# Kernel tuning notes

Hardware: AMD Instinct MI355X
Metric: run time of the kernel (lower is better)

Reference implementation:

```python
import jax, jax.numpy as jnp
import numpy as np

LR = 1e-3  # Oja online learning rate
B, D, H, O = 2048, 784, 256, 10


def setup_inputs() -> dict:
    key = jax.random.key(0)
    k0, k1, k2, k3, k4 = jax.random.split(key, 5)
    x = jax.random.normal(k0, (B, D), dtype=jnp.float32)
    whiten_mean = 0.1 * jax.random.normal(k1, (D,), dtype=jnp.float32)
    # whitening matrix ~ identity + small perturbation (well-conditioned)
    whiten_mat = jnp.eye(D, dtype=jnp.float32) + 0.01 * jax.random.normal(k2, (D, D), dtype=jnp.float32)
    oja_W = (1.0 / np.sqrt(D)) * jax.random.normal(k3, (H, D), dtype=jnp.float32)
    readout_W = (1.0 / np.sqrt(H)) * jax.random.normal(k4, (O, H), dtype=jnp.float32)
    readout_b = jnp.zeros((O,), dtype=jnp.float32)
    return {"x": x, "whiten_mean": whiten_mean, "whiten_mat": whiten_mat,
            "oja_W": oja_W, "readout_W": readout_W, "readout_b": readout_b}


def reference(x, whiten_mean, whiten_mat, oja_W, readout_W, readout_b):
    # Whitening transform per sample: x_w = M (x - mu)
    xw = (x - whiten_mean) @ whiten_mat.T  # [B, D]

    # Sequential Oja online updates: y_i = W_i x_i ; W_{i+1} = W_i + lr*(y x^T - (y y^T) W_i)
    def step(W, xi):
        y = W @ xi                                        # [H]
        W_new = W + LR * (jnp.outer(y, xi) - jnp.outer(y, y) @ W)
        return W_new, y

    _, feats = jax.lax.scan(step, oja_W, xw)              # feats: [B, H]

    # dropout(p=0.2) in eval mode is identity; then ReLU and linear readout
    feats = jax.nn.relu(feats)
    logits = feats @ readout_W.T + readout_b              # [B, O]
    return logits
```

## Files before the change

### kernel.cpp

```cpp
#include <hip/hip_runtime.h>

#define LRATE 1e-3f
static constexpr int Bn = 2048;
static constexpr int Dn = 784;
static constexpr int Hn = 256;
static constexpr int On = 10;
static constexpr int Cc = 64;
static constexpr int NCHUNK = Bn / Cc;

static constexpr int AS = 68;
static constexpr int YS = 260;
static constexpr int MSZ = 64 * AS;

__device__ __forceinline__ float red4(float s) {
  s += __uint_as_float(__builtin_amdgcn_mov_dpp(__float_as_uint(s), 0xB1, 0xF, 0xF, true));
  s += __uint_as_float(__builtin_amdgcn_mov_dpp(__float_as_uint(s), 0x4E, 0xF, 0xF, true));
  return s;
}

__global__ __launch_bounds__(256) void whiten_kernel(
    const float* __restrict__ x, const float* __restrict__ mean,
    const float* __restrict__ Mw, float* __restrict__ xw)
{
  __shared__ __align__(16) float As[16][64];
  __shared__ __align__(16) float Bs[16][64];
  const int tid = threadIdx.x;
  const int b0 = blockIdx.x * 64;
  const int d0 = blockIdx.y * 64;
  const int mrow = tid >> 2;
  const int kq = (tid & 3) << 2;
  const int ty = tid >> 4, tx = tid & 15;

  float acc[4][4];
#pragma unroll
  for (int i = 0; i < 4; ++i)
#pragma unroll
    for (int j = 0; j < 4; ++j) acc[i][j] = 0.f;

  for (int k0 = 0; k0 < Dn; k0 += 16) {
    __syncthreads();
    {
      const float4 av = *(const float4*)&x[(b0 + mrow) * Dn + k0 + kq];
      const float4 mv = *(const float4*)&mean[k0 + kq];
      As[kq + 0][mrow] = av.x - mv.x;
      As[kq + 1][mrow] = av.y - mv.y;
      As[kq + 2][mrow] = av.z - mv.z;
      As[kq + 3][mrow] = av.w - mv.w;
      float4 bv = make_float4(0.f, 0.f, 0.f, 0.f);
      if (d0 + mrow < Dn) bv = *(const float4*)&Mw[(d0 + mrow) * Dn + k0 + kq];
      Bs[kq + 0][mrow] = bv.x;
      Bs[kq + 1][mrow] = bv.y;
      Bs[kq + 2][mrow] = bv.z;
      Bs[kq + 3][mrow] = bv.w;
    }
    __syncthreads();
#pragma unroll
    for (int k = 0; k < 16; ++k) {
      const float4 a = *(const float4*)&As[k][ty << 2];
      const float4 b = *(const float4*)&Bs[k][tx << 2];
      acc[0][0] += a.x * b.x; acc[0][1] += a.x * b.y; acc[0][2] += a.x * b.z; acc[0][3] += a.x * b.w;
      acc[1][0] += a.y * b.x; acc[1][1] += a.y * b.y; acc[1][2] += a.y * b.z; acc[1][3] += a.y * b.w;
      acc[2][0] += a.z * b.x; acc[2][1] += a.z * b.y; acc[2][2] += a.z * b.z; acc[2][3] += a.z * b.w;
      acc[3][0] += a.w * b.x; acc[3][1] += a.w * b.y; acc[3][2] += a.w * b.z; acc[3][3] += a.w * b.w;
    }
  }
  const int col = d0 + (tx << 2);
  if (col < Dn) {
#pragma unroll
    for (int i = 0; i < 4; ++i) {
      const int row = b0 + (ty << 2) + i;
      *(float4*)&xw[row * Dn + col] =
          make_float4(acc[i][0], acc[i][1], acc[i][2], acc[i][3]);
    }
  }
}

__global__ __launch_bounds__(256) void sgram_kernel(
    const float* __restrict__ xw, float* __restrict__ S_all)
{
  __shared__ __align__(16) float Xs[64 * 396];
  const int t = threadIdx.x;
  const int c = blockIdx.x;
  const float* xc = xw + (size_t)c * Cc * Dn;
  const int ti = t >> 4, tj = t & 15;
  float acc[4][4];
#pragma unroll
  for (int a = 0; a < 4; ++a)
#pragma unroll
    for (int b = 0; b < 4; ++b) acc[a][b] = 0.f;

  for (int pass = 0; pass < 2; ++pass) {
    __syncthreads();
    for (int e4 = t; e4 < 64 * 98; e4 += 256) {
      const int r = e4 / 98, c4 = e4 - r * 98;
      *(float4*)&Xs[r * 396 + 4 * c4] =
          *(const float4*)&xc[r * Dn + pass * 392 + 4 * c4];
    }
    __syncthreads();
    for (int k4 = 0; k4 < 98; ++k4) {
      float4 A[4], Bv[4];
#pragma unroll
      for (int a = 0; a < 4; ++a) A[a] = *(const float4*)&Xs[(4 * ti + a) * 396 + 4 * k4];
#pragma unroll
      for (int b = 0; b < 4; ++b) Bv[b] = *(const float4*)&Xs[(4 * tj + b) * 396 + 4 * k4];
#pragma unroll
      for (int a = 0; a < 4; ++a)
#pragma unroll
        for (int b = 0; b < 4; ++b)
          acc[a][b] += A[a].x * Bv[b].x + A[a].y * Bv[b].y + A[a].z * Bv[b].z + A[a].w * Bv[b].w;
    }
  }
  float* Sc = S_all + (size_t)c * Cc * Cc;
#pragma unroll
  for (int a = 0; a < 4; ++a)
#pragma unroll
    for (int b = 0; b < 4; ++b)
      Sc[(4 * ti + a) * Cc + 4 * tj + b] = acc[a][b];
}

__global__ __launch_bounds__(256) void yhat_kernel(
    const float* __restrict__ xc, const float* __restrict__ W,
    float* __restrict__ yhat)
{
  const int t = threadIdx.x;
  const int r = t & 63, hh = t >> 6;
  const int h = blockIdx.x * 4 + hh;
  const float4* xr = (const float4*)&xc[r * Dn];
  const float4* wr = (const float4*)&W[h * Dn];
  float acc = 0.f;
#pragma unroll 4
  for (int f = 0; f < 196; ++f) {
    const float4 a = xr[f], b = wr[f];
    acc += a.x * b.x + a.y * b.y + a.z * b.z + a.w * b.w;
  }
  yhat[r * Hn + h] = acc;
}

__global__ __launch_bounds__(256, 1) void seq_kernel(
    const float* __restrict__ yhat_g, const float* __restrict__ S_g,
    float* __restrict__ feats_c, float* __restrict__ beta_g)
{
  __shared__ __align__(16) float lds[8 * MSZ + 1872];
  float* Gy  = lds + 0 * MSZ;
  float* AlT = lds + 1 * MSZ;
  float* BeT = lds + 2 * MSZ;
  float* GuT = lds + 3 * MSZ;
  float* Qs  = lds + 4 * MSZ;
  float* Ts  = lds + 5 * MSZ;
  float* Ss  = lds + 6 * MSZ;
  float* Al  = lds + 7 * MSZ;
  float* VOb = lds + 8 * MSZ;
  float* VMb = VOb + 4 * AS;
  float* GVo = VMb + 4 * AS;
  float* Pk  = GVo + 16;

  const int t = threadIdx.x;
  const int k = t >> 2, qr = t & 3;
  const int m0q = qr * 16;

  for (int e4 = t; e4 < 5 * MSZ / 4; e4 += 256)
    *(float4*)&lds[4 * e4] = make_float4(0.f, 0.f, 0.f, 0.f);
  for (int e4 = t; e4 < 1024; e4 += 256) {
    const int r = e4 >> 4, c4 = e4 & 15;
    *(float4*)&Ss[r * AS + 4 * c4] = ((const float4*)S_g)[e4];
  }
  {
    const int ti = t >> 4, tj = t & 15;
    float acc[4][4];
#pragma unroll
    for (int a = 0; a < 4; ++a)
#pragma unroll
      for (int b = 0; b < 4; ++b) acc[a][b] = 0.f;
    for (int k4 = 0; k4 < 64; ++k4) {
      float4 A[4], Bv[4];
#pragma unroll
      for (int a = 0; a < 4; ++a) A[a] = *(const float4*)&yhat_g[(4 * ti + a) * Hn + 4 * k4];
#pragma unroll
      for (int b = 0; b < 4; ++b) Bv[b] = *(const float4*)&yhat_g[(4 * tj + b) * Hn + 4 * k4];
#pragma unroll
      for (int a = 0; a < 4; ++a)
#pragma unroll
        for (int b = 0; b < 4; ++b)
          acc[a][b] += A[a].x * Bv[b].x + A[a].y * Bv[b].y + A[a].z * Bv[b].z + A[a].w * Bv[b].w;
    }
#pragma unroll
    for (int a = 0; a < 4; ++a)
#pragma unroll
      for (int b = 0; b < 4; ++b)
        Ts[(4 * ti + a) * AS + 4 * tj + b] = acc[a][b];
  }
  __syncthreads();

  __builtin_amdgcn_s_setprio(1);

  for (int b = 0; b < Cc / 4; ++b) {
    const int b0 = 4 * b;
    const int wseg = (b0 + 15) >> 4;
    const int o4 = qr * wseg;

    float4 gyS[4], atS[4], qS[4];
    {
      const float4* gyp = (const float4*)&Gy[k * AS] + o4;
      const float4* atp = (const float4*)&AlT[k * AS] + o4;
      const float4* qp  = (const float4*)&Qs[k * AS] + o4;
#pragma unroll
      for (int f = 0; f < 4; ++f)
        if (f < wseg) { gyS[f] = gyp[f]; atS[f] = atp[f]; qS[f] = qp[f]; }
    }
    float og[4], oq[4], oa[4], grow[4];
#pragma unroll
    for (int s = 0; s < 4; ++s) {
      const float4* pR = (const float4*)&GuT[(b0 + s) * AS] + o4;
      float g0 = 0.f, g1 = 0.f, g2 = 0.f, g3 = 0.f;
      float a0 = 0.f, a1 = 0.f, a2 = 0.f, a3 = 0.f;
      float w0 = 0.f, w1 = 0.f, w2 = 0.f, w3 = 0.f;
#pragma unroll
      for (int f = 0; f < 4; ++f)
        if (f < wseg) {
          const float4 p = pR[f];
          g0 += p.x * gyS[f].x; g1 += p.y * gyS[f].y; g2 += p.z * gyS[f].z; g3 += p.w * gyS[f].w;
          a0 += p.x * atS[f].x; a1 += p.y * atS[f].y; a2 += p.z * atS[f].z; a3 += p.w * atS[f].w;
          w0 += p.x * qS[f].x;  w1 += p.y * qS[f].y;  w2 += p.z * qS[f].z;  w3 += p.w * qS[f].w;
        }
      og[s] = red4((g0 + g1) + (g2 + g3));
      oa[s] = red4((a0 + a1) + (a2 + a3));
      oq[s] = red4((w0 + w1) + (w2 + w3));
      grow[s] = Gy[(b0 + s) * AS + k];
    }
    if (qr == 0)      *(float4*)&Pk[k * 20 + 0] = make_float4(og[0], og[1], og[2], og[3]);
    else if (qr == 1) *(float4*)&Pk[k * 20 + 4] = make_float4(oq[0], oq[1], oq[2], oq[3]);
    else if (qr == 2) *(float4*)&Pk[k * 20 + 8] = make_float4(oa[0], oa[1], oa[2], oa[3]);
    else {
      float vo[4];
#pragma unroll
      for (int s = 0; s < 4; ++s) vo[s] = grow[s] + LRATE * oq[s];
      *(float4*)&Pk[k * 20 + 12] = make_float4(vo[0], vo[1], vo[2], vo[3]);
#pragma unroll
      for (int s = 0; s < 4; ++s) VOb[s * AS + k] = vo[s];
    }
    __syncthreads();

    if (t < 64) {
      const int pr = t >> 2;
      const int sp = pr >> 2, s2 = pr & 3;
      const int q2 = t & 3;
      const float4* gr = (const float4*)&GuT[(b0 + sp) * AS] + q2 * wseg;
      const float4* vr = (const float4*)&VOb[s2 * AS] + q2 * wseg;
      float d0 = 0.f, d1 = 0.f, d2 = 0.f, d3 = 0.f;
#pragma unroll
      for (int f = 0; f < 4; ++f)
        if (f < wseg) {
          const float4 g = gr[f], v = vr[f];
          d0 += g.x * v.x; d1 += g.y * v.y; d2 += g.z * v.z; d3 += g.w * v.w;
        }
      const float d = red4((d0 + d1) + (d2 + d3));
      if (q2 == 0) GVo[pr] = d;
    }
    __syncthreads();

    float T8[4][4], S8v[4][4], OG8[4][4], OQ8[4][4], GV8[4][4];
#pragma unroll
    for (int j = 0; j < 4; ++j) {
      const float4 t4 = *(const float4*)&Ts[(b0 + j) * AS + b0];
      T8[j][0] = t4.x; T8[j][1] = t4.y; T8[j][2] = t4.z; T8[j][3] = t4.w;
      const float4 s4 = *(const float4*)&Ss[(b0 + j) * AS + b0];
      S8v[j][0] = s4.x; S8v[j][1] = s4.y; S8v[j][2] = s4.z; S8v[j][3] = s4.w;
      const float4 g4 = *(const float4*)&Pk[(b0 + j) * 20 + 0];
      OG8[0][j] = g4.x; OG8[1][j] = g4.y; OG8[2][j] = g4.z; OG8[3][j] = g4.w;
      const float4 q4 = *(const float4*)&Pk[(b0 + j) * 20 + 4];
      OQ8[0][j] = q4.x; OQ8[1][j] = q4.y; OQ8[2][j] = q4.z; OQ8[3][j] = q4.w;
      const float4 v4 = ((const float4*)GVo)[j];
      GV8[j][0] = v4.x; GV8[j][1] = v4.y; GV8[j][2] = v4.z; GV8[j][3] = v4.w;
    }
    float G8[4][4], V8[4][4], U8[4][4], W8[4][4], Qd[4];
#pragma unroll
    for (int j = 0; j < 4; ++j) {
      G8[0][j] = T8[0][j] + LRATE * OG8[0][j];
      V8[0][j] = 0.f;
      W8[j][0] = GV8[j][0];
    }
#pragma unroll
    for (int j = 0; j < 4; ++j) U8[0][j] = S8v[0][j] - G8[0][j] - LRATE * W8[j][0];
    Qd[0] = G8[0][0] + LRATE * W8[0][0];
    {
      const float p0 = U8[0][1];
#pragma unroll
      for (int j = 0; j < 4; ++j) G8[1][j] = T8[1][j] + LRATE * (OG8[1][j] + p0 * G8[0][j]);
      V8[1][0] = G8[0][1] + LRATE * (OQ8[1][0] + p0 * Qd[0]);
      V8[1][1] = V8[1][2] = V8[1][3] = 0.f;
#pragma unroll
      for (int j = 0; j < 4; ++j) W8[j][1] = GV8[j][1] + LRATE * (p0 * W8[j][0]);
#pragma unroll
      for (int j = 0; j < 4; ++j)
        U8[1][j] = S8v[1][j] - G8[1][j] - LRATE * (W8[j][1] + V8[1][0] * U8[0][j]);
      Qd[1] = G8[1][1] + LRATE * (W8[1][1] + p0 * V8[1][0]);
    }
    {
      const float p0 = U8[0][2], p1 = U8[1][2];
#pragma unroll
      for (int j = 0; j < 4; ++j)
        G8[2][j] = T8[2][j] + LRATE * (OG8[2][j] + p0 * G8[0][j] + p1 * G8[1][j]);
      V8[2][0] = G8[0][2] + LRATE * (OQ8[2][0] + p0 * Qd[0] + p1 * V8[1][0]);
      V8[2][1] = G8[1][2] + LRATE * (OQ8[2][1] + p1 * Qd[1]);
      V8[2][2] = V8[2][3] = 0.f;
#pragma unroll
      for (int j = 0; j < 4; ++j) W8[j][2] = GV8[j][2] + LRATE * (p0 * W8[j][0] + p1 * W8[j][1]);
#pragma unroll
      for (int j = 0; j < 4; ++j)
        U8[2][j] = S8v[2][j] - G8[2][j] -
                   LRATE * (W8[j][2] + V8[2][0] * U8[0][j] + V8[2][1] * U8[1][j]);
      Qd[2] = G8[2][2] + LRATE * (W8[2][2] + p0 * V8[2][0] + p1 * V8[2][1]);
    }
    {
      const float p0 = U8[0][3], p1 = U8[1][3], p2 = U8[2][3];
#pragma unroll
      for (int j = 0; j < 4; ++j)
        G8[3][j] = T8[3][j] + LRATE * (OG8[3][j] + p0 * G8[0][j] + p1 * G8[1][j] + p2 * G8[2][j]);
      V8[3][0] = G8[0][3] + LRATE * (OQ8[3][0] + p0 * Qd[0] + p1 * V8[1][0] + p2 * V8[2][0]);
      V8[3][1] = G8[1][3] + LRATE * (OQ8[3][1] + p1 * Qd[1] + p2 * V8[2][1]);
      V8[3][2] = G8[2][3] + LRATE * (OQ8[3][2] + p2 * Qd[2]);
      V8[3][3] = 0.f;
#pragma unroll
      for (int j = 0; j < 4; ++j)
        W8[j][3] = GV8[j][3] + LRATE * (p0 * W8[j][0] + p1 * W8[j][1] + p2 * W8[j][2]);
#pragma unroll
      for (int j = 0; j < 4; ++j)
        U8[3][j] = S8v[3][j] - G8[3][j] -
                   LRATE * (W8[j][3] + V8[3][0] * U8[0][j] + V8[3][1] * U8[1][j] +
                            V8[3][2] * U8[2][j]);
      Qd[3] = G8[3][3] + LRATE * (W8[3][3] + p0 * V8[3][0] + p1 * V8[3][1] + p2 * V8[3][2]);
    }

    float TsK[4], OGk[4], OAk[4], VOk[4];
    {
      const float4 tk4 = *(const float4*)&Ts[k * AS + b0];
      TsK[0] = tk4.x; TsK[1] = tk4.y; TsK[2] = tk4.z; TsK[3] = tk4.w;
      const float4 og4 = *(const float4*)&Pk[k * 20 + 0];
      OGk[0] = og4.x; OGk[1] = og4.y; OGk[2] = og4.z; OGk[3] = og4.w;
      const float4 oa4 = *(const float4*)&Pk[k * 20 + 8];
      OAk[0] = oa4.x; OAk[1] = oa4.y; OAk[2] = oa4.z; OAk[3] = oa4.w;
      const float4 vo4 = *(const float4*)&Pk[k * 20 + 12];
      VOk[0] = vo4.x; VOk[1] = vo4.y; VOk[2] = vo4.z; VOk[3] = vo4.w;
    }
    float gy[4], aI[4], vm[4];
    gy[0] = TsK[0] + LRATE * OGk[0];
    { const float a = LRATE * OAk[0]; aI[0] = (k < b0) ? a : ((k == b0) ? 1.f : 0.f); }
    vm[0] = (k < b0) ? VOk[0] : 0.f;
    {
      const float p0 = U8[0][1];
      gy[1] = TsK[1] + LRATE * (OGk[1] + p0 * gy[0]);
      const float a = LRATE * (OAk[1] + p0 * aI[0]);
      aI[1] = (k < b0 + 1) ? a : ((k == b0 + 1) ? 1.f : 0.f);
      const float vt0 = (k == b0) ? Qd[0] : vm[0];
      float v = VOk[1] + LRATE * (p0 * vt0);
      if (k == b0) v += G8[0][1];
      vm[1] = (k < b0 + 1) ? v : 0.f;
    }
    {
      const float p0 = U8[0][2], p1 = U8[1][2];
      gy[2] = TsK[2] + LRATE * (OGk[2] + p0 * gy[0] + p1 * gy[1]);
      const float a = LRATE * (OAk[2] + p0 * aI[0] + p1 * aI[1]);
      aI[2] = (k < b0 + 2) ? a : ((k == b0 + 2) ? 1.f : 0.f);
      const float vt0 = (k == b0) ? Qd[0] : vm[0];
      const float vt1 = (k == b0 + 1) ? Qd[1] : vm[1];
      float v = VOk[2] + LRATE * (p0 * vt0 + p1 * vt1);
      if (k == b0) v += G8[0][2];
      else if (k == b0 + 1) v += G8[1][2];
      vm[2] = (k < b0 + 2) ? v : 0.f;
    }
    {
      const float p0 = U8[0][3], p1 = U8[1][3], p2 = U8[2][3];
      gy[3] = TsK[3] + LRATE * (OGk[3] + p0 * gy[0] + p1 * gy[1] + p2 * gy[2]);
      const float a = LRATE * (OAk[3] + p0 * aI[0] + p1 * aI[1] + p2 * aI[2]);
      aI[3] = (k < b0 + 3) ? a : ((k == b0 + 3) ? 1.f : 0.f);
      const float vt0 = (k == b0) ? Qd[0] : vm[0];
      const float vt1 = (k == b0 + 1) ? Qd[1] : vm[1];
      const float vt2 = (k == b0 + 2) ? Qd[2] : vm[2];
      float v = VOk[3] + LRATE * (p0 * vt0 + p1 * vt1 + p2 * vt2);
      if (k == b0) v += G8[0][3];
      else if (k == b0 + 1) v += G8[1][3];
      else if (k == b0 + 2) v += G8[2][3];
      vm[3] = (k < b0 + 3) ? v : 0.f;
    }
    float qw[4];
#pragma unroll
    for (int s = 0; s < 4; ++s) qw[s] = (k == b0 + s) ? Qd[s] : vm[s];
    if (qr == 0) {
      *(float4*)&Gy[k * AS + b0] = make_float4(gy[0], gy[1], gy[2], gy[3]);
#pragma unroll
      for (int s = 0; s < 4; ++s) Qs[(b0 + s) * AS + k] = qw[s];
    } else if (qr == 1) {
      *(float4*)&AlT[k * AS + b0] = make_float4(aI[0], aI[1], aI[2], aI[3]);
      *(float4*)&Qs[k * AS + b0] = make_float4(qw[0], qw[1], qw[2], qw[3]);
    } else if (qr == 2) {
#pragma unroll
      for (int s = 0; s < 4; ++s) Al[(b0 + s) * AS + k] = aI[s];
#pragma unroll
      for (int s = 0; s < 4; ++s) VMb[s * AS + k] = (k < b0) ? vm[s] : 0.f;
    }
    __syncthreads();

    float4 beS[4], guS[4];
    {
      const float4* bep = (const float4*)&BeT[k * AS] + o4;
      const float4* gup = (const float4*)&GuT[k * AS] + o4;
#pragma unroll
      for (int f = 0; f < 4; ++f)
        if (f < wseg) { beS[f] = bep[f]; guS[f] = gup[f]; }
    }
    float bO[4], gO[4];
#pragma unroll
    for (int s = 0; s < 4; ++s) {
      const float4* vmr = (const float4*)&VMb[s * AS] + o4;
      float b0a = 0.f, b1a = 0.f, b2a = 0.f, b3a = 0.f;
      float u0 = 0.f, u1 = 0.f, u2 = 0.f, u3 = 0.f;
#pragma unroll
      for (int f = 0; f < 4; ++f)
        if (f < wseg) {
          const float4 v = vmr[f];
          b0a += v.x * beS[f].x; b1a += v.y * beS[f].y; b2a += v.z * beS[f].z; b3a += v.w * beS[f].w;
          u0 += v.x * guS[f].x; u1 += v.y * guS[f].y; u2 += v.z * guS[f].z; u3 += v.w * guS[f].w;
        }
      bO[s] = red4((b0a + b1a) + (b2a + b3a));
      gO[s] = red4((u0 + u1) + (u2 + u3));
    }
    float SsK[4];
    {
      const float4 sk4 = *(const float4*)&Ss[k * AS + b0];
      SsK[0] = sk4.x; SsK[1] = sk4.y; SsK[2] = sk4.z; SsK[3] = sk4.w;
    }
    float bI[4], gu[4];
    {
      const float bb = -LRATE * bO[0];
      bI[0] = (k < b0) ? bb : ((k == b0) ? 1.f : 0.f);
      gu[0] = SsK[0] - gy[0] - LRATE * gO[0];
    }
    {
      const float bb = -LRATE * (bO[1] + V8[1][0] * bI[0]);
      bI[1] = (k < b0 + 1) ? bb : ((k == b0 + 1) ? 1.f : 0.f);
      gu[1] = SsK[1] - gy[1] - LRATE * (gO[1] + V8[1][0] * gu[0]);
    }
    {
      const float bb = -LRATE * (bO[2] + V8[2][0] * bI[0] + V8[2][1] * bI[1]);
      bI[2] = (k < b0 + 2) ? bb : ((k == b0 + 2) ? 1.f : 0.f);
      gu[2] = SsK[2] - gy[2] - LRATE * (gO[2] + V8[2][0] * gu[0] + V8[2][1] * gu[1]);
    }
    {
      const float bb = -LRATE * (bO[3] + V8[3][0] * bI[0] + V8[3][1] * bI[1] + V8[3][2] * bI[2]);
      bI[3] = (k < b0 + 3) ? bb : ((k == b0 + 3) ? 1.f : 0.f);
      gu[3] = SsK[3] - gy[3] -
              LRATE * (gO[3] + V8[3][0] * gu[0] + V8[3][1] * gu[1] + V8[3][2] * gu[2]);
    }
    if (qr == 0) {
      *(float4*)&GuT[k * AS + b0] = make_float4(gu[0], gu[1], gu[2], gu[3]);
    } else if (qr == 1) {
      *(float4*)&BeT[k * AS + b0] = make_float4(bI[0], bI[1], bI[2], bI[3]);
    }
    __syncthreads();
  }

  __builtin_amdgcn_s_setprio(0);

  {
    const int r = t >> 2, q = t & 3;
#pragma unroll
    for (int kk = 0; kk < 16; ++kk) {
      const int kcol = q * 16 + kk;
      beta_g[r * 64 + kcol] = BeT[kcol * AS + r];
    }
  }
  __syncthreads();

  for (int e4 = t; e4 < 4096; e4 += 256) {
    const int r = e4 >> 6, c4 = e4 & 63;
    *(float4*)&lds[r * YS + 4 * c4] = ((const float4*)yhat_g)[e4];
  }
  __syncthreads();

  {
    const int r = k;
    const int m0q4 = m0q * 4;
    float a[64];
#pragma unroll
    for (int f = 0; f < 16; ++f) {
      const float4 av = *(const float4*)&Al[r * AS + 4 * f];
      a[4 * f + 0] = av.x; a[4 * f + 1] = av.y;
      a[4 * f + 2] = av.z; a[4 * f + 3] = av.w;
    }
    float4 acc[16];
#pragma unroll
    for (int f = 0; f < 16; ++f) acc[f] = make_float4(0.f, 0.f, 0.f, 0.f);
#pragma unroll
    for (int m4 = 0; m4 < 16; ++m4) {
      const float av0 = a[4 * m4 + 0], av1 = a[4 * m4 + 1];
      const float av2 = a[4 * m4 + 2], av3 = a[4 * m4 + 3];
      const float4* y0 = (const float4*)&lds[(4 * m4 + 0) * YS + m0q4];
      const float4* y1 = (const float4*)&lds[(4 * m4 + 1) * YS + m0q4];
      const float4* y2 = (const float4*)&lds[(4 * m4 + 2) * YS + m0q4];
      const float4* y3 = (const float4*)&lds[(4 * m4 + 3) * YS + m0q4];
#pragma unroll
      for (int f = 0; f < 16; ++f) {
        const float4 z0 = y0[f], z1 = y1[f], z2 = y2[f], z3 = y3[f];
        acc[f].x += av0 * z0.x + av1 * z1.x + av2 * z2.x + av3 * z3.x;
        acc[f].y += av0 * z0.y + av1 * z1.y + av2 * z2.y + av3 * z3.y;
        acc[f].z += av0 * z0.z + av1 * z1.z + av2 * z2.z + av3 * z3.z;
        acc[f].w += av0 * z0.w + av1 * z1.w + av2 * z2.w + av3 * z3.w;
      }
    }
    float4* dst = (float4*)&feats_c[r * Hn + m0q4];
#pragma unroll
    for (int f = 0; f < 16; ++f) dst[f] = acc[f];
  }
}

__global__ __launch_bounds__(256, 1) void upd_kernel(
    const float* __restrict__ xc, const float* __restrict__ Yg,
    const float* __restrict__ beta_g, float* __restrict__ W)
{
  __shared__ __align__(16) float Yl[64 * YS];
  __shared__ __align__(16) float bl[64 * AS];
  __shared__ __align__(16) float WlT[8 * YS];
  __shared__ __align__(16) float XT[8 * 64];
  __shared__ __align__(16) float VT[8 * 64];
  __shared__ __align__(16) float UT[8 * 64];
  const int t = threadIdx.x;
  const int d0 = blockIdx.x * 8;

  {
    const int r = t >> 2, qr = t & 3;
    const float4* src = (const float4*)&Yg[r * Hn + qr * 64];
    float4* dst = (float4*)&Yl[r * YS + qr * 64];
#pragma unroll
    for (int f = 0; f < 16; ++f) dst[f] = src[f];
  }
#pragma unroll
  for (int f = 0; f < 4; ++f) {
    const int e4 = t + 256 * f;
    const int r = e4 >> 4, c4 = e4 & 15;
    *(float4*)&bl[r * AS + 4 * c4] = ((const float4*)beta_g)[e4];
  }
  {
    const float4* wsrc = (const float4*)&W[t * Dn + d0];
    const float4 w0 = wsrc[0], w1 = wsrc[1];
    WlT[0 * YS + t] = w0.x; WlT[1 * YS + t] = w0.y; WlT[2 * YS + t] = w0.z; WlT[3 * YS + t] = w0.w;
    WlT[4 * YS + t] = w1.x; WlT[5 * YS + t] = w1.y; WlT[6 * YS + t] = w1.z; WlT[7 * YS + t] = w1.w;
  }
  if (t < 64) {
    const float4* xsrc = (const float4*)&xc[t * Dn + d0];
    const float4 x0 = xsrc[0], x1 = xsrc[1];
    XT[0 * 64 + t] = x0.x; XT[1 * 64 + t] = x0.y; XT[2 * 64 + t] = x0.z; XT[3 * 64 + t] = x0.w;
    XT[4 * 64 + t] = x1.x; XT[5 * 64 + t] = x1.y; XT[6 * 64 + t] = x1.z; XT[7 * 64 + t] = x1.w;
  }
  __syncthreads();
  const int r = t & 63, da = t >> 6, db = da + 4;
  {
    float va = XT[da * 64 + r], vb = XT[db * 64 + r];
    const float4* yrow = (const float4*)&Yl[r * YS];
    const float4* wa = (const float4*)&WlT[da * YS];
    const float4* wb = (const float4*)&WlT[db * YS];
#pragma unroll 8
    for (int f = 0; f < 64; ++f) {
      const float4 y = yrow[f], A = wa[f], Bv = wb[f];
      va -= y.x * A.x + y.y * A.y + y.z * A.z + y.w * A.w;
      vb -= y.x * Bv.x + y.y * Bv.y + y.z * Bv.z + y.w * Bv.w;
    }
    VT[da * 64 + r] = va; VT[db * 64 + r] = vb;
  }
  __syncthreads();
  {
    float ua = 0.f, ub = 0.f;
    const float4* br = (const float4*)&bl[r * AS];
    const float4* vta = (const float4*)&VT[da * 64];
    const float4* vtb = (const float4*)&VT[db * 64];
#pragma unroll
    for (int f = 0; f < 16; ++f) {
      const float4 b = br[f], A = vta[f], Bv = vtb[f];
      ua += b.x * A.x + b.y * A.y + b.z * A.z + b.w * A.w;
      ub += b.x * Bv.x + b.y * Bv.y + b.z * Bv.z + b.w * Bv.w;
    }
    UT[da * 64 + r] = ua; UT[db * 64 + r] = ub;
  }
  __syncthreads();
  {
    float wacc[8];
#pragma unroll
    for (int dj = 0; dj < 8; ++dj) wacc[dj] = 0.f;
    for (int r4 = 0; r4 < 16; ++r4) {
      float4 u[8];
#pragma unroll
      for (int dj = 0; dj < 8; ++dj) u[dj] = *(const float4*)&UT[dj * 64 + 4 * r4];
      const float y0 = Yl[(4 * r4 + 0) * YS + t];
      const float y1 = Yl[(4 * r4 + 1) * YS + t];
      const float y2 = Yl[(4 * r4 + 2) * YS + t];
      const float y3 = Yl[(4 * r4 + 3) * YS + t];
#pragma unroll
      for (int dj = 0; dj < 8; ++dj)
        wacc[dj] += y0 * u[dj].x + y1 * u[dj].y + y2 * u[dj].z + y3 * u[dj].w;
    }
    float4 o0, o1;
    o0.x = WlT[0 * YS + t] + LRATE * wacc[0];
    o0.y = WlT[1 * YS + t] + LRATE * wacc[1];
    o0.z = WlT[2 * YS + t] + LRATE * wacc[2];
    o0.w = WlT[3 * YS + t] + LRATE * wacc[3];
    o1.x = WlT[4 * YS + t] + LRATE * wacc[4];
    o1.y = WlT[5 * YS + t] + LRATE * wacc[5];
    o1.z = WlT[6 * YS + t] + LRATE * wacc[6];
    o1.w = WlT[7 * YS + t] + LRATE * wacc[7];
    float4* wdst = (float4*)&W[t * Dn + d0];
    wdst[0] = o0; wdst[1] = o1;
  }
}

__global__ __launch_bounds__(256) void readout_kernel(
    const float* __restrict__ feats, const float* __restrict__ R,
    const float* __restrict__ bias, float* __restrict__ out)
{
  const int g = blockIdx.x * 256 + threadIdx.x;
  if (g >= Bn * On) return;
  const int b = g / On;
  const int o = g - b * On;
  const float* f = feats + b * Hn;
  const float* r = R + o * Hn;
  float acc = bias[o];
#pragma unroll 8
  for (int h = 0; h < Hn; ++h) acc += fmaxf(f[h], 0.f) * r[h];
  out[g] = acc;
}

extern "C" void kernel_launch(void* const* d_in, const int* in_sizes, int n_in,
                              void* d_out, int out_size, void* d_ws, size_t ws_size,
                              hipStream_t stream) {
  const float* x    = (const float*)d_in[0];
  const float* mean = (const float*)d_in[1];
  const float* Mw   = (const float*)d_in[2];
  const float* W0   = (const float*)d_in[3];
  const float* R    = (const float*)d_in[4];
  const float* bias = (const float*)d_in[5];
  float* out = (float*)d_out;

  float* p = (float*)d_ws;
  float* xw     = p;  p += (size_t)Bn * Dn;
  float* feats  = p;  p += (size_t)Bn * Hn;
  float* W_dyn  = p;  p += (size_t)Hn * Dn;
  float* S_all  = p;  p += (size_t)NCHUNK * Cc * Cc;
  float* yhat   = p;  p += (size_t)Cc * Hn;
  float* beta_g = p;  p += (size_t)Cc * Cc;
  (void)ws_size; (void)n_in; (void)in_sizes; (void)out_size;

  whiten_kernel<<<dim3(Bn / 64, (Dn + 63) / 64), 256, 0, stream>>>(x, mean, Mw, xw);
  sgram_kernel<<<NCHUNK, 256, 0, stream>>>(xw, S_all);
  hipMemcpyAsync(W_dyn, W0, (size_t)Hn * Dn * sizeof(float),
                 hipMemcpyDeviceToDevice, stream);

  for (int c = 0; c < NCHUNK; ++c) {
    const float* xc = xw + (size_t)c * Cc * Dn;
    float* feats_c  = feats + (size_t)c * Cc * Hn;
    yhat_kernel<<<64, 256, 0, stream>>>(xc, W_dyn, yhat);
    seq_kernel<<<1, 256, 0, stream>>>(yhat, S_all + (size_t)c * Cc * Cc,
                                      feats_c, beta_g);
    upd_kernel<<<98, 256, 0, stream>>>(xc, feats_c, beta_g, W_dyn);
  }

  readout_kernel<<<(Bn * On + 255) / 256, 256, 0, stream>>>(feats, R, bias, out);
}
```

Measured before the change: 4.839 ms.

## Split seq kernel into Gram, recurrence, and feature-projection kernels

Moves the yhat Gram-matrix computation out of the single-block seq kernel into its own tgram kernel, which stages yhat in LDS instead of reading it strided from global memory. Moves the final feats = Al·yhat projection into a separate 4-block kernel. The seq kernel now only loads T and S, runs the recurrence and writes Al and beta. Each chunk now needs two more kernel launches and extra global round trips for T and Al, and the new kernels are still very small, so launch overhead may cancel the gain.

Result: faster. 3.995 ms (-17.4%).

```diff
diff --git a/kernel.cpp b/kernel.cpp
--- a/kernel.cpp
+++ b/kernel.cpp
@@ -136,9 +136,43 @@
   yhat[r * Hn + h] = acc;
 }
 
+__global__ __launch_bounds__(256, 1) void tgram_kernel(
+    const float* __restrict__ yhat_g, float* __restrict__ Ts_g)
+{
+  __shared__ __align__(16) float Ys[64 * YS];
+  const int t = threadIdx.x;
+  for (int e4 = t; e4 < 4096; e4 += 256) {
+    const int r = e4 >> 6, c4 = e4 & 63;
+    *(float4*)&Ys[r * YS + 4 * c4] = ((const float4*)yhat_g)[e4];
+  }
+  __syncthreads();
+  const int ti = t >> 4, tj = t & 15;
+  float acc[4][4];
+#pragma unroll
+  for (int a = 0; a < 4; ++a)
+#pragma unroll
+    for (int b = 0; b < 4; ++b) acc[a][b] = 0.f;
+  for (int k4 = 0; k4 < 64; ++k4) {
+    float4 A[4], Bv[4];
+#pragma unroll
+    for (int a = 0; a < 4; ++a) A[a] = *(const float4*)&Ys[(4 * ti + a) * YS + 4 * k4];
+#pragma unroll
+    for (int b = 0; b < 4; ++b) Bv[b] = *(const float4*)&Ys[(4 * tj + b) * YS + 4 * k4];
+#pragma unroll
+    for (int a = 0; a < 4; ++a)
+#pragma unroll
+      for (int b = 0; b < 4; ++b)
+        acc[a][b] += A[a].x * Bv[b].x + A[a].y * Bv[b].y + A[a].z * Bv[b].z + A[a].w * Bv[b].w;
+  }
+#pragma unroll
+  for (int a = 0; a < 4; ++a)
+    *(float4*)&Ts_g[(4 * ti + a) * 64 + 4 * tj] =
+        make_float4(acc[a][0], acc[a][1], acc[a][2], acc[a][3]);
+}
+
 __global__ __launch_bounds__(256, 1) void seq_kernel(
-    const float* __restrict__ yhat_g, const float* __restrict__ S_g,
-    float* __restrict__ feats_c, float* __restrict__ beta_g)
+    const float* __restrict__ Ts_g, const float* __restrict__ S_g,
+    float* __restrict__ Al_g, float* __restrict__ beta_g)
 {
   __shared__ __align__(16) float lds[8 * MSZ + 1872];
   float* Gy  = lds + 0 * MSZ;
@@ -156,38 +190,13 @@
 
   const int t = threadIdx.x;
   const int k = t >> 2, qr = t & 3;
-  const int m0q = qr * 16;
 
   for (int e4 = t; e4 < 5 * MSZ / 4; e4 += 256)
     *(float4*)&lds[4 * e4] = make_float4(0.f, 0.f, 0.f, 0.f);
   for (int e4 = t; e4 < 1024; e4 += 256) {
     const int r = e4 >> 4, c4 = e4 & 15;
     *(float4*)&Ss[r * AS + 4 * c4] = ((const float4*)S_g)[e4];
-  }
-  {
-    const int ti = t >> 4, tj = t & 15;
-    float acc[4][4];
-#pragma unroll
-    for (int a = 0; a < 4; ++a)
-#pragma unroll
-      for (int b = 0; b < 4; ++b) acc[a][b] = 0.f;
-    for (int k4 = 0; k4 < 64; ++k4) {
-      float4 A[4], Bv[4];
-#pragma unroll
-      for (int a = 0; a < 4; ++a) A[a] = *(const float4*)&yhat_g[(4 * ti + a) * Hn + 4 * k4];
-#pragma unroll
-      for (int b = 0; b < 4; ++b) Bv[b] = *(const float4*)&yhat_g[(4 * tj + b) * Hn + 4 * k4];
-#pragma unroll
-      for (int a = 0; a < 4; ++a)
-#pragma unroll
-        for (int b = 0; b < 4; ++b)
-          acc[a][b] += A[a].x * Bv[b].x + A[a].y * Bv[b].y + A[a].z * Bv[b].z + A[a].w * Bv[b].w;
-    }
-#pragma unroll
-    for (int a = 0; a < 4; ++a)
-#pragma unroll
-      for (int b = 0; b < 4; ++b)
-        Ts[(4 * ti + a) * AS + 4 * tj + b] = acc[a][b];
+    *(float4*)&Ts[r * AS + 4 * c4] = ((const float4*)Ts_g)[e4];
   }
   __syncthreads();
 
@@ -469,48 +478,48 @@
       beta_g[r * 64 + kcol] = BeT[kcol * AS + r];
     }
   }
-  __syncthreads();
-
-  for (int e4 = t; e4 < 4096; e4 += 256) {
-    const int r = e4 >> 6, c4 = e4 & 63;
-    *(float4*)&lds[r * YS + 4 * c4] = ((const float4*)yhat_g)[e4];
-  }
-  __syncthreads();
-
-  {
-    const int r = k;
-    const int m0q4 = m0q * 4;
-    float a[64];
+  for (int e4 = t; e4 < 1024; e4 += 256) {
+    const int r = e4 >> 4, c4 = e4 & 15;
+    ((float4*)Al_g)[e4] = *(const float4*)&Al[r * AS + 4 * c4];
+  }
+}
+
+__global__ __launch_bounds__(64) void feats_kernel(
+    const float* __restrict__ Al_g, const float* __restrict__ yhat_g,
+    float* __restrict__ feats_c)
+{
+  const int r = threadIdx.x;
+  const int m0q4 = blockIdx.x * 64;
+  float a[64];
+#pragma unroll
+  for (int f = 0; f < 16; ++f) {
+    const float4 av = *(const float4*)&Al_g[r * 64 + 4 * f];
+    a[4 * f + 0] = av.x; a[4 * f + 1] = av.y;
+    a[4 * f + 2] = av.z; a[4 * f + 3] = av.w;
+  }
+  float4 acc[16];
+#pragma unroll
+  for (int f = 0; f < 16; ++f) acc[f] = make_float4(0.f, 0.f, 0.f, 0.f);
+#pragma unroll
+  for (int m4 = 0; m4 < 16; ++m4) {
+    const float av0 = a[4 * m4 + 0], av1 = a[4 * m4 + 1];
+    const float av2 = a[4 * m4 + 2], av3 = a[4 * m4 + 3];
+    const float4* y0 = (const float4*)&yhat_g[(4 * m4 + 0) * Hn + m0q4];
+    const float4* y1 = (const float4*)&yhat_g[(4 * m4 + 1) * Hn + m0q4];
+    const float4* y2 = (const float4*)&yhat_g[(4 * m4 + 2) * Hn + m0q4];
+    const float4* y3 = (const float4*)&yhat_g[(4 * m4 + 3) * Hn + m0q4];
 #pragma unroll
     for (int f = 0; f < 16; ++f) {
-      const float4 av = *(const float4*)&Al[r * AS + 4 * f];
-      a[4 * f + 0] = av.x; a[4 * f + 1] = av.y;
-      a[4 * f + 2] = av.z; a[4 * f + 3] = av.w;
-    }
-    float4 acc[16];
-#pragma unroll
-    for (int f = 0; f < 16; ++f) acc[f] = make_float4(0.f, 0.f, 0.f, 0.f);
-#pragma unroll
-    for (int m4 = 0; m4 < 16; ++m4) {
-      const float av0 = a[4 * m4 + 0], av1 = a[4 * m4 + 1];
-      const float av2 = a[4 * m4 + 2], av3 = a[4 * m4 + 3];
-      const float4* y0 = (const float4*)&lds[(4 * m4 + 0) * YS + m0q4];
-      const float4* y1 = (const float4*)&lds[(4 * m4 + 1) * YS + m0q4];
-      const float4* y2 = (const float4*)&lds[(4 * m4 + 2) * YS + m0q4];
-      const float4* y3 = (const float4*)&lds[(4 * m4 + 3) * YS + m0q4];
-#pragma unroll
-      for (int f = 0; f < 16; ++f) {
-        const float4 z0 = y0[f], z1 = y1[f], z2 = y2[f], z3 = y3[f];
-        acc[f].x += av0 * z0.x + av1 * z1.x + av2 * z2.x + av3 * z3.x;
-        acc[f].y += av0 * z0.y + av1 * z1.y + av2 * z2.y + av3 * z3.y;
-        acc[f].z += av0 * z0.z + av1 * z1.z + av2 * z2.z + av3 * z3.z;
-        acc[f].w += av0 * z0.w + av1 * z1.w + av2 * z2.w + av3 * z3.w;
-      }
-    }
-    float4* dst = (float4*)&feats_c[r * Hn + m0q4];
-#pragma unroll
-    for (int f = 0; f < 16; ++f) dst[f] = acc[f];
-  }
+      const float4 z0 = y0[f], z1 = y1[f], z2 = y2[f], z3 = y3[f];
+      acc[f].x += av0 * z0.x + av1 * z1.x + av2 * z2.x + av3 * z3.x;
+      acc[f].y += av0 * z0.y + av1 * z1.y + av2 * z2.y + av3 * z3.y;
+      acc[f].z += av0 * z0.z + av1 * z1.z + av2 * z2.z + av3 * z3.z;
+      acc[f].w += av0 * z0.w + av1 * z1.w + av2 * z2.w + av3 * z3.w;
+    }
+  }
+  float4* dst = (float4*)&feats_c[r * Hn + m0q4];
+#pragma unroll
+  for (int f = 0; f < 16; ++f) dst[f] = acc[f];
 }
 
 __global__ __launch_bounds__(256, 1) void upd_kernel(
@@ -645,6 +654,8 @@
   float* S_all  = p;  p += (size_t)NCHUNK * Cc * Cc;
   float* yhat   = p;  p += (size_t)Cc * Hn;
   float* beta_g = p;  p += (size_t)Cc * Cc;
+  float* Ts_g   = p;  p += (size_t)Cc * Cc;
+  float* Al_g   = p;  p += (size_t)Cc * Cc;
   (void)ws_size; (void)n_in; (void)in_sizes; (void)out_size;
 
   whiten_kernel<<<dim3(Bn / 64, (Dn + 63) / 64), 256, 0, stream>>>(x, mean, Mw, xw);
@@ -656,8 +667,10 @@
     const float* xc = xw + (size_t)c * Cc * Dn;
     float* feats_c  = feats + (size_t)c * Cc * Hn;
     yhat_kernel<<<64, 256, 0, stream>>>(xc, W_dyn, yhat);
-    seq_kernel<<<1, 256, 0, stream>>>(yhat, S_all + (size_t)c * Cc * Cc,
-                                      feats_c, beta_g);
+    tgram_kernel<<<1, 256, 0, stream>>>(yhat, Ts_g);
+    seq_kernel<<<1, 256, 0, stream>>>(Ts_g, S_all + (size_t)c * Cc * Cc,
+                                      Al_g, beta_g);
+    feats_kernel<<<4, 64, 0, stream>>>(Al_g, yhat, feats_c);
     upd_kernel<<<98, 256, 0, stream>>>(xc, feats_c, beta_g, W_dyn);
   }
 
```
